# Kernel tuning notes

Measured on AMD Instinct MI355X. Metric: run time of the kernel, lower is better.

Reference implementation:

```python
import jax, jax.numpy as jnp
import numpy as np

EMBED_DIM = 2048
NUM_HEADS = 16
HEAD_DIM = EMBED_DIM // NUM_HEADS  # 128
D_K = 128
SCALE = 1.0 / float(np.sqrt(HEAD_DIM))
LAYER_DEPTH = 6 / 12  # amrpa_layer_idx / n_amrpa_layers
BATCH, SEQ = 2, 2048


def setup_inputs() -> dict:
    key = jax.random.key(0)
    ks = jax.random.split(key, 8)
    return {
        "hidden_states": jax.random.normal(ks[0], (BATCH, SEQ, EMBED_DIM), jnp.float32),
        "c_attn_w": jax.random.normal(ks[1], (EMBED_DIM, 3 * EMBED_DIM), jnp.float32) * 0.02,
        "c_attn_b": jax.random.normal(ks[2], (3 * EMBED_DIM,), jnp.float32) * 0.02,
        "c_proj_w": jax.random.normal(ks[3], (EMBED_DIM, EMBED_DIM), jnp.float32) * 0.02,
        "c_proj_b": jax.random.normal(ks[4], (EMBED_DIM,), jnp.float32) * 0.02,
        "cam_gate": jax.random.normal(ks[5], (D_K,), jnp.float32) * 0.1,
        "cam_w0": jax.random.normal(ks[6], (1,), jnp.float32),
        "cam_w1": jax.random.normal(ks[7], (1,), jnp.float32),
    }


def reference(hidden_states, c_attn_w, c_attn_b, c_proj_w, c_proj_b, cam_gate, cam_w0, cam_w1):
    # GPT2 Conv1D-style fused QKV projection: [B,S,3E]
    qkv = hidden_states @ c_attn_w + c_attn_b
    Q, K, V = jnp.split(qkv, 3, axis=2)  # each [B,S,E]
    # NOTE: faithful to source — attention over the FULL embed dim (no head split),
    # scaled by 1/sqrt(head_dim); causal mask is computed but never applied upstream.
    attn_scores = jnp.einsum('bse,bte->bst', Q, K) * SCALE  # [B,S,S]

    # CAM: sliced low-rank channels
    Q_cam, K_cam, V_cam = Q[:, :, :D_K], K[:, :, :D_K], V[:, :, :D_K]
    # base attention map computed under no_grad in the original
    base_A = jax.lax.stop_gradient(
        jax.nn.softmax(jnp.einsum('bsd,btd->bst', Q_cam, K_cam) * SCALE, axis=-1))
    layer_weight = jax.nn.sigmoid(cam_w0[0] + cam_w1[0] * LAYER_DEPTH)
    cam_ctx = jnp.einsum('bst,btd->bsd', base_A, V_cam)            # [B,S,d_k]
    cam_bias = jnp.einsum('bsd,btd->bst', jnp.tanh(cam_ctx * cam_gate), K_cam)
    cam_bias = cam_bias * (SCALE * layer_weight)                   # cam_mask is all-ones

    final_attn = jax.nn.softmax(attn_scores + cam_bias, axis=-1)
    context = jnp.einsum('bst,bte->bse', final_attn, V)            # [B,S,E]
    output = context @ c_proj_w + c_proj_b                         # resid_dropout is identity (eval)
    return output
```

## Files before the change

### kernel.cpp

```cpp
#include <hip/hip_runtime.h>
#include <hip/hip_bf16.h>

typedef unsigned short u16;
typedef __attribute__((ext_vector_type(8))) __bf16 bf16x8;
typedef __attribute__((ext_vector_type(4))) float f32x4;
typedef __attribute__((ext_vector_type(4))) unsigned short u16x4;

#define SCALE_QK 0.08838834764831845f

__device__ __forceinline__ u16 f2bf(float x) {
  union { float f; unsigned u; } v; v.f = x;
  unsigned r = v.u + 0x7fffu + ((v.u >> 16) & 1u);
  return (u16)(r >> 16);
}

__device__ __forceinline__ void gload_lds16(const u16* g, u16* l) {
  __builtin_amdgcn_global_load_lds(
      (const __attribute__((address_space(1))) unsigned*)g,
      (__attribute__((address_space(3))) unsigned*)l, 16, 0, 0);
}

__device__ __forceinline__ void wgbar() {
  asm volatile("" ::: "memory");
  __builtin_amdgcn_s_barrier();
  asm volatile("" ::: "memory");
}

template<bool OUT_BF16, bool HAS_BIAS>
__global__ __launch_bounds__(512, 2)
void gemm256(const u16* __restrict__ A, int lda, long sA,
             const u16* __restrict__ B, int ldb, long sB,
             void* __restrict__ Cv, int ldc, long sC,
             int K, float scale, const float* __restrict__ scale_ptr,
             const float* __restrict__ bias, int nbx)
{
  extern __shared__ u16 lds[];
  const int bz = blockIdx.z;
  const u16* Ap = A + (long)bz * sA;
  const u16* Bp = B + (long)bz * sB;

  const int nwg = gridDim.x;
  const int orig = blockIdx.x;
  const int q = nwg >> 3, rr = nwg & 7;
  const int xcd = orig & 7, lp = orig >> 3;
  const int wg = (xcd < rr ? xcd * (q + 1) : rr * (q + 1) + (xcd - rr) * q) + lp;
  const int bx = wg % nbx, by = wg / nbx;
  const long m0 = (long)by * 256, n0 = (long)bx * 256;

  const int tid = threadIdx.x;
  const int wid = tid >> 6, lane = tid & 63;
  const int wm = wid >> 2, wn = wid & 3;
  const int rl = lane & 15, g = lane >> 4;

  int offA[8], offB[4];
#pragma unroll
  for (int i = 0; i < 8; ++i) {
    const int row = wm * 128 + i * 16 + rl;
    offA[i] = row * 32 + ((g ^ ((row >> 1) & 3)) << 3);
  }
#pragma unroll
  for (int j = 0; j < 4; ++j) {
    const int row = wn * 64 + j * 16 + rl;
    offB[j] = row * 32 + ((g ^ ((row >> 1) & 3)) << 3);
  }

  const int rA = tid >> 2;
  const int colsw = (((lane & 3) ^ ((rA >> 1) & 3)) << 3);
  const u16* srcA0 = Ap + (m0 + rA) * (long)lda + colsw;
  const u16* srcA1 = Ap + (m0 + rA + 128) * (long)lda + colsw;
  const u16* srcB0 = Bp + (n0 + rA) * (long)ldb + colsw;
  const u16* srcB1 = Bp + (n0 + rA + 128) * (long)ldb + colsw;
  const int dL0 = wid * 512, dL1 = wid * 512 + 4096;

  const int NT = K >> 5;

#pragma unroll 1
  for (int t = 0; t < 3; ++t) {
    u16* bufp = lds + (t & 3) * 16384;
    gload_lds16(srcA0 + t * 32, bufp + dL0);
    gload_lds16(srcA1 + t * 32, bufp + dL1);
    gload_lds16(srcB0 + t * 32, bufp + 8192 + dL0);
    gload_lds16(srcB1 + t * 32, bufp + 8192 + dL1);
  }

  f32x4 acc[8][4];
#pragma unroll
  for (int i = 0; i < 8; ++i)
#pragma unroll
    for (int j = 0; j < 4; ++j) acc[i][j] = (f32x4){0.f, 0.f, 0.f, 0.f};

#pragma unroll 1
  for (int t = 0; t < NT; ++t) {
    const u16* bA = lds + (t & 3) * 16384;
    const u16* bB = bA + 8192;
    const int pre = t + 3;
    const bool doPre = pre < NT;
    u16* pP = lds + (pre & 3) * 16384;
    const int rem = NT - 1 - t;
    if (rem >= 2)      asm volatile("s_waitcnt vmcnt(8)" ::: "memory");
    else if (rem == 1) asm volatile("s_waitcnt vmcnt(4)" ::: "memory");
    else               asm volatile("s_waitcnt vmcnt(0)" ::: "memory");
    wgbar();

    bf16x8 av[4], bv_[4];
#pragma unroll
    for (int i = 0; i < 4; ++i) av[i] = *(const bf16x8*)(bA + offA[i]);
#pragma unroll
    for (int j = 0; j < 4; ++j) bv_[j] = *(const bf16x8*)(bB + offB[j]);
    if (doPre) {
      gload_lds16(srcA0 + pre * 32, pP + dL0);
      gload_lds16(srcA1 + pre * 32, pP + dL1);
    }
    wgbar();
    __builtin_amdgcn_s_setprio(1);
#pragma unroll
    for (int i = 0; i < 4; ++i)
#pragma unroll
      for (int j = 0; j < 4; ++j)
        acc[i][j] = __builtin_amdgcn_mfma_f32_16x16x32_bf16(av[i], bv_[j], acc[i][j], 0, 0, 0);
    __builtin_amdgcn_s_setprio(0);

#pragma unroll
    for (int i = 0; i < 4; ++i) av[i] = *(const bf16x8*)(bA + offA[i + 4]);
    if (doPre) {
      gload_lds16(srcB0 + pre * 32, pP + 8192 + dL0);
      gload_lds16(srcB1 + pre * 32, pP + 8192 + dL1);
    }
    wgbar();
    __builtin_amdgcn_s_setprio(1);
#pragma unroll
    for (int i = 0; i < 4; ++i)
#pragma unroll
      for (int j = 0; j < 4; ++j)
        acc[i + 4][j] = __builtin_amdgcn_mfma_f32_16x16x32_bf16(av[i], bv_[j], acc[i + 4][j], 0, 0, 0);
    __builtin_amdgcn_s_setprio(0);
  }

  float sc = scale;
  if (scale_ptr) sc *= scale_ptr[0];
  const int r0 = (lane >> 4) << 2;
  const int cL = lane & 15;
#pragma unroll
  for (int i = 0; i < 8; ++i) {
#pragma unroll
    for (int j = 0; j < 4; ++j) {
      const long row = m0 + wm * 128 + i * 16 + r0;
      const long col = n0 + wn * 64 + j * 16 + cL;
      float bvs = 0.f;
      if (HAS_BIAS) bvs = bias[col];
      if (OUT_BF16) {
        u16* Cp = (u16*)Cv + (long)bz * sC;
#pragma unroll
        for (int r = 0; r < 4; ++r)
          Cp[(row + r) * ldc + col] = f2bf(acc[i][j][r] * sc + bvs);
      } else {
        float* Cp = (float*)Cv + (long)bz * sC;
#pragma unroll
        for (int r = 0; r < 4; ++r)
          Cp[(row + r) * ldc + col] = acc[i][j][r] * sc + bvs;
      }
    }
  }
}

template<bool OUT_BF16, bool ACCUM, bool HAS_BIAS>
__global__ __launch_bounds__(256)
void gemm_bt(const u16* __restrict__ A, int lda, long sA,
             const u16* __restrict__ B, int ldb, long sB,
             void* __restrict__ Cv, int ldc, long sC,
             int K, float scale, const float* __restrict__ scale_ptr,
             const float* __restrict__ bias)
{
  __shared__ u16 As[128 * 64];
  __shared__ u16 Bs[128 * 64];
  const int bz   = blockIdx.z;
  const u16* Ap  = A + (long)bz * sA;
  const u16* Bp  = B + (long)bz * sB;
  const int tid  = threadIdx.x;
  const int wid  = tid >> 6;
  const int lane = tid & 63;
  const long m0  = (long)blockIdx.y * 128;
  const long n0  = (long)blockIdx.x * 128;
  const int lrow = lane >> 3;
  const int lk   = (lane & 7) << 3;
  const int wr   = wid >> 1, wc = wid & 1;

  f32x4 acc[4][4];
#pragma unroll
  for (int i = 0; i < 4; ++i)
#pragma unroll
    for (int j = 0; j < 4; ++j) acc[i][j] = (f32x4){0.f, 0.f, 0.f, 0.f};

  for (int k0 = 0; k0 < K; k0 += 64) {
#pragma unroll
    for (int c4 = 0; c4 < 4; ++c4) {
      const int chunk = (wid << 2) + c4;
      gload_lds16(Ap + (m0 + (chunk << 3) + lrow) * lda + k0 + lk, &As[chunk << 9]);
      gload_lds16(Bp + (n0 + (chunk << 3) + lrow) * ldb + k0 + lk, &Bs[chunk << 9]);
    }
    __syncthreads();
#pragma unroll
    for (int kk = 0; kk < 2; ++kk) {
      bf16x8 af[4], bfr[4];
      const int kof   = (kk << 5) + ((lane >> 4) << 3);
      const int rbase = lane & 15;
#pragma unroll
      for (int i = 0; i < 4; ++i)
        af[i] = *(const bf16x8*)&As[(((wr << 6) + (i << 4) + rbase) << 6) + kof];
#pragma unroll
      for (int j = 0; j < 4; ++j)
        bfr[j] = *(const bf16x8*)&Bs[(((wc << 6) + (j << 4) + rbase) << 6) + kof];
#pragma unroll
      for (int i = 0; i < 4; ++i)
#pragma unroll
        for (int j = 0; j < 4; ++j)
          acc[i][j] = __builtin_amdgcn_mfma_f32_16x16x32_bf16(af[i], bfr[j], acc[i][j], 0, 0, 0);
    }
    __syncthreads();
  }

  float sc = scale;
  if (scale_ptr) sc *= scale_ptr[0];
  const int r0 = (lane >> 4) << 2;
  const int cL = lane & 15;
#pragma unroll
  for (int i = 0; i < 4; ++i) {
#pragma unroll
    for (int j = 0; j < 4; ++j) {
      const long row = m0 + (wr << 6) + (i << 4) + r0;
      const long col = n0 + (wc << 6) + (j << 4) + cL;
      float bv = 0.f;
      if (HAS_BIAS) bv = bias[col];
      if (OUT_BF16) {
        u16* Cp = (u16*)Cv + (long)bz * sC;
#pragma unroll
        for (int r = 0; r < 4; ++r)
          Cp[(row + r) * ldc + col] = f2bf(acc[i][j][r] * sc + bv);
      } else {
        float* Cp = (float*)Cv + (long)bz * sC;
#pragma unroll
        for (int r = 0; r < 4; ++r) {
          float v = acc[i][j][r] * sc + bv;
          if (ACCUM) Cp[(row + r) * ldc + col] += v;
          else       Cp[(row + r) * ldc + col] = v;
        }
      }
    }
  }
}

__global__ __launch_bounds__(256)
void gemm_bt_splitk(const u16* __restrict__ A, int lda, long sA,
                    const u16* __restrict__ B, int ldb, long sB,
                    float* __restrict__ C, int ldc, long sC,
                    int Kslice, float scale)
{
  __shared__ u16 As[128 * 64];
  __shared__ u16 Bs[128 * 64];
  const int ks = blockIdx.z & 7;
  const int bz = blockIdx.z >> 3;
  const u16* Ap  = A + (long)bz * sA + ks * Kslice;
  const u16* Bp  = B + (long)bz * sB + ks * Kslice;
  const int tid  = threadIdx.x;
  const int wid  = tid >> 6;
  const int lane = tid & 63;
  const long m0  = (long)blockIdx.y * 128;
  const long n0  = (long)blockIdx.x * 128;
  const int lrow = lane >> 3;
  const int lk   = (lane & 7) << 3;
  const int wr   = wid >> 1, wc = wid & 1;

  f32x4 acc[4][4];
#pragma unroll
  for (int i = 0; i < 4; ++i)
#pragma unroll
    for (int j = 0; j < 4; ++j) acc[i][j] = (f32x4){0.f, 0.f, 0.f, 0.f};

  for (int k0 = 0; k0 < Kslice; k0 += 64) {
#pragma unroll
    for (int c4 = 0; c4 < 4; ++c4) {
      const int chunk = (wid << 2) + c4;
      gload_lds16(Ap + (m0 + (chunk << 3) + lrow) * lda + k0 + lk, &As[chunk << 9]);
      gload_lds16(Bp + (n0 + (chunk << 3) + lrow) * ldb + k0 + lk, &Bs[chunk << 9]);
    }
    __syncthreads();
#pragma unroll
    for (int kk = 0; kk < 2; ++kk) {
      bf16x8 af[4], bfr[4];
      const int kof   = (kk << 5) + ((lane >> 4) << 3);
      const int rbase = lane & 15;
#pragma unroll
      for (int i = 0; i < 4; ++i)
        af[i] = *(const bf16x8*)&As[(((wr << 6) + (i << 4) + rbase) << 6) + kof];
#pragma unroll
      for (int j = 0; j < 4; ++j)
        bfr[j] = *(const bf16x8*)&Bs[(((wc << 6) + (j << 4) + rbase) << 6) + kof];
#pragma unroll
      for (int i = 0; i < 4; ++i)
#pragma unroll
        for (int j = 0; j < 4; ++j)
          acc[i][j] = __builtin_amdgcn_mfma_f32_16x16x32_bf16(af[i], bfr[j], acc[i][j], 0, 0, 0);
    }
    __syncthreads();
  }

  const int r0 = (lane >> 4) << 2;
  const int cL = lane & 15;
  float* Cp = C + (long)bz * sC;
#pragma unroll
  for (int i = 0; i < 4; ++i) {
#pragma unroll
    for (int j = 0; j < 4; ++j) {
      const long row = m0 + (wr << 6) + (i << 4) + r0;
      const long col = n0 + (wc << 6) + (j << 4) + cL;
#pragma unroll
      for (int r = 0; r < 4; ++r)
        atomicAdd(&Cp[(row + r) * ldc + col], acc[i][j][r] * scale);
    }
  }
}

__global__ __launch_bounds__(256)
void softmax_rows2048(const float* __restrict__ src, u16* __restrict__ dst) {
  const long row = blockIdx.x;
  const float4* s = (const float4*)(src + row * 2048);
  const int tid = threadIdx.x;
  float4 a = s[tid * 2], b = s[tid * 2 + 1];
  float m = fmaxf(fmaxf(fmaxf(a.x, a.y), fmaxf(a.z, a.w)),
                  fmaxf(fmaxf(b.x, b.y), fmaxf(b.z, b.w)));
#pragma unroll
  for (int o = 32; o > 0; o >>= 1) m = fmaxf(m, __shfl_xor(m, o));
  __shared__ float redm[4];
  __shared__ float reds[4];
  if ((tid & 63) == 0) redm[tid >> 6] = m;
  __syncthreads();
  m = fmaxf(fmaxf(redm[0], redm[1]), fmaxf(redm[2], redm[3]));
  float e[8];
  e[0] = __expf(a.x - m); e[1] = __expf(a.y - m); e[2] = __expf(a.z - m); e[3] = __expf(a.w - m);
  e[4] = __expf(b.x - m); e[5] = __expf(b.y - m); e[6] = __expf(b.z - m); e[7] = __expf(b.w - m);
  float sum = e[0] + e[1] + e[2] + e[3] + e[4] + e[5] + e[6] + e[7];
#pragma unroll
  for (int o = 32; o > 0; o >>= 1) sum += __shfl_xor(sum, o);
  if ((tid & 63) == 0) reds[tid >> 6] = sum;
  __syncthreads();
  sum = reds[0] + reds[1] + reds[2] + reds[3];
  const float inv = 1.f / sum;
  u16x4 o1 = { f2bf(e[0] * inv), f2bf(e[1] * inv), f2bf(e[2] * inv), f2bf(e[3] * inv) };
  u16x4 o2 = { f2bf(e[4] * inv), f2bf(e[5] * inv), f2bf(e[6] * inv), f2bf(e[7] * inv) };
  u16x4* d = (u16x4*)(dst + row * 2048);
  d[tid * 2]     = o1;
  d[tid * 2 + 1] = o2;
}

__global__ void transpose_f32_to_bf16(const float* __restrict__ src, u16* __restrict__ dst,
                                      int R, int C) {
  __shared__ float t[32][33];
  const int c0 = blockIdx.x * 32, r0 = blockIdx.y * 32;
  const int tx = threadIdx.x, ty = threadIdx.y;
#pragma unroll
  for (int i = 0; i < 4; ++i)
    t[ty + i * 8][tx] = src[(long)(r0 + ty + i * 8) * C + c0 + tx];
  __syncthreads();
#pragma unroll
  for (int i = 0; i < 4; ++i)
    dst[(long)(c0 + ty + i * 8) * R + r0 + tx] = f2bf(t[tx][ty + i * 8]);
}

__global__ void transpose_bf16_batched(const u16* __restrict__ src, int ss, long sbat,
                                       u16* __restrict__ dst, int ds, long dbat) {
  __shared__ u16 t[32][33];
  const u16* s = src + (long)blockIdx.z * sbat;
  u16* d = dst + (long)blockIdx.z * dbat;
  const int c0 = blockIdx.x * 32, r0 = blockIdx.y * 32;
  const int tx = threadIdx.x, ty = threadIdx.y;
#pragma unroll
  for (int i = 0; i < 4; ++i)
    t[ty + i * 8][tx] = s[(long)(r0 + ty + i * 8) * ss + c0 + tx];
  __syncthreads();
#pragma unroll
  for (int i = 0; i < 4; ++i)
    d[(long)(c0 + ty + i * 8) * ds + r0 + tx] = t[tx][ty + i * 8];
}

__global__ __launch_bounds__(256)
void convert_f32_to_bf16(const float* __restrict__ src, u16* __restrict__ dst, long n4) {
  long i = (long)blockIdx.x * 256 + threadIdx.x;
  if (i < n4) {
    float4 v = ((const float4*)src)[i];
    *(u16x4*)(dst + i * 4) = (u16x4){ f2bf(v.x), f2bf(v.y), f2bf(v.z), f2bf(v.w) };
  }
}

__global__ __launch_bounds__(256)
void cam_tanh_kernel(const float* __restrict__ ctx, const float* __restrict__ gate,
                     u16* __restrict__ out, int n) {
  int i = blockIdx.x * 256 + threadIdx.x;
  if (i < n) {
    int d = i & 127;
    out[i] = f2bf(tanhf(ctx[i] * gate[d]));
  }
}

__global__ __launch_bounds__(256)
void zero_f32(float* __restrict__ p, int n) {
  int i = blockIdx.x * 256 + threadIdx.x;
  if (i < n) p[i] = 0.f;
}

__global__ void calc_lw_kernel(const float* w0, const float* w1, float* lw) {
  *lw = 1.f / (1.f + __expf(-(w0[0] + 0.5f * w1[0])));
}

extern "C" void kernel_launch(void* const* d_in, const int* in_sizes, int n_in,
                              void* d_out, int out_size, void* d_ws, size_t ws_size,
                              hipStream_t stream) {
  const float* hs       = (const float*)d_in[0];
  const float* c_attn_w = (const float*)d_in[1];
  const float* c_attn_b = (const float*)d_in[2];
  const float* c_proj_w = (const float*)d_in[3];
  const float* c_proj_b = (const float*)d_in[4];
  const float* cam_gate = (const float*)d_in[5];
  const float* cam_w0   = (const float*)d_in[6];
  const float* cam_w1   = (const float*)d_in[7];
  float* out = (float*)d_out;

  char* w = (char*)d_ws;
  float* lw      = (float*)(w + 0);
  u16*   hs_b    = (u16*)(w + 256);
  u16*   waT_b   = (u16*)(w + 256 + 16777216UL);
  u16*   wpT_b   = (u16*)(w + 256 + 41943040UL);
  u16*   qkv_b   = (u16*)(w + 256 + 50331648UL);
  u16*   vT_b    = (u16*)(w + 256 + 100663296UL);
  float* scoresF = (float*)(w + 256 + 117440512UL);
  float* camS    = (float*)(w + 256 + 150994944UL);
  float* ctxF    = (float*)(w + 256 + 184549376UL);
  u16*   camT_b  = (u16*)(w + 256 + 186646528UL);
  u16* baseA_b = hs_b;
  u16* P_b     = (u16*)camS;
  u16* ctxE_b  = (u16*)scoresF;

  dim3 b256(256);

  {
    auto* kfn = gemm256<true, true>;
    hipFuncSetAttribute((const void*)kfn, hipFuncAttributeMaxDynamicSharedMemorySize, 131072);
  }

  calc_lw_kernel<<<dim3(1), dim3(1), 0, stream>>>(cam_w0, cam_w1, lw);
  convert_f32_to_bf16<<<dim3(8192), b256, 0, stream>>>(hs, hs_b, 2097152L);
  transpose_f32_to_bf16<<<dim3(192, 64), dim3(32, 8), 0, stream>>>(c_attn_w, waT_b, 2048, 6144);
  transpose_f32_to_bf16<<<dim3(64, 64), dim3(32, 8), 0, stream>>>(c_proj_w, wpT_b, 2048, 2048);

  gemm256<true, true><<<dim3(384, 1, 1), dim3(512), 131072, stream>>>(
      hs_b, 2048, 0L, waT_b, 2048, 0L, qkv_b, 6144, 0L,
      2048, 1.f, nullptr, c_attn_b, 24);

  transpose_bf16_batched<<<dim3(64, 64, 2), dim3(32, 8), 0, stream>>>(
      qkv_b + 4096, 6144, 2048L * 6144, vT_b, 2048, 2048L * 2048);

  gemm_bt<false, false, false><<<dim3(16, 16, 2), b256, 0, stream>>>(
      qkv_b, 6144, 2048L * 6144, qkv_b + 2048, 6144, 2048L * 6144,
      scoresF, 2048, 2048L * 2048, 2048, SCALE_QK, nullptr, nullptr);

  gemm_bt<false, false, false><<<dim3(16, 16, 2), b256, 0, stream>>>(
      qkv_b, 6144, 2048L * 6144, qkv_b + 2048, 6144, 2048L * 6144,
      camS, 2048, 2048L * 2048, 128, SCALE_QK, nullptr, nullptr);

  softmax_rows2048<<<dim3(4096), b256, 0, stream>>>(camS, baseA_b);

  zero_f32<<<dim3(2048), b256, 0, stream>>>(ctxF, 524288);
  gemm_bt_splitk<<<dim3(1, 16, 16), b256, 0, stream>>>(
      baseA_b, 2048, 2048L * 2048, vT_b, 2048, 2048L * 2048,
      ctxF, 128, 2048L * 128, 256, 1.f);

  cam_tanh_kernel<<<dim3(2048), b256, 0, stream>>>(ctxF, cam_gate, camT_b, 524288);

  gemm_bt<false, true, false><<<dim3(16, 16, 2), b256, 0, stream>>>(
      camT_b, 128, 2048L * 128, qkv_b + 2048, 6144, 2048L * 6144,
      scoresF, 2048, 2048L * 2048, 128, SCALE_QK, lw, nullptr);

  softmax_rows2048<<<dim3(4096), b256, 0, stream>>>(scoresF, P_b);

  gemm_bt<true, false, false><<<dim3(16, 16, 2), b256, 0, stream>>>(
      P_b, 2048, 2048L * 2048, vT_b, 2048, 2048L * 2048,
      ctxE_b, 2048, 2048L * 2048, 2048, 1.f, nullptr, nullptr);

  gemm_bt<false, false, true><<<dim3(16, 32, 1), b256, 0, stream>>>(
      ctxE_b, 2048, 0L, wpT_b, 2048, 0L, out, 2048, 0L,
      2048, 1.f, nullptr, c_proj_b);
}
```

Measured before the change: 399.8 us.

## Move attention GEMMs to 256-tile pipelined kernel and fuse CAM bias into scores

Rewrites the 256x256 GEMM as a double-buffered pipeline with 64-wide K steps, staging loads in sub-phases interleaved with MFMA work. The same kernel now handles QK^T, PV and the output projection, which previously used the smaller 128-tile kernel. The CAM bias is folded into the score GEMM as a second K segment (tanh ctx times K), with the layer weight pre-multiplied in the tanh kernel. This removes the separate accumulate pass and a read-modify-write of the fp32 score matrix. In exchange, the 2048x2048 GEMMs launch only 128 workgroups each, which may underfill the GPU.

Measured after the change: 392.4 us. About the same (-1.8%).

```diff
diff --git a/kernel.cpp b/kernel.cpp
--- a/kernel.cpp
+++ b/kernel.cpp
@@ -20,30 +20,25 @@
       (__attribute__((address_space(3))) unsigned*)l, 16, 0, 0);
 }
 
-__device__ __forceinline__ void wgbar() {
-  asm volatile("" ::: "memory");
-  __builtin_amdgcn_s_barrier();
-  asm volatile("" ::: "memory");
-}
-
-template<bool OUT_BF16, bool HAS_BIAS>
+#define CFENCE() asm volatile("" ::: "memory")
+
+template<bool OUT_BF16, bool HAS_BIAS, bool TWO_SEG>
 __global__ __launch_bounds__(512, 2)
-void gemm256(const u16* __restrict__ A, int lda, long sA,
-             const u16* __restrict__ B, int ldb, long sB,
-             void* __restrict__ Cv, int ldc, long sC,
-             int K, float scale, const float* __restrict__ scale_ptr,
-             const float* __restrict__ bias, int nbx)
+void gemm256_8ph(const u16* __restrict__ A1, int lda1, long sA1,
+                 const u16* __restrict__ B1, int ldb1, long sB1, int K1,
+                 const u16* __restrict__ A2, int lda2, long sA2,
+                 const u16* __restrict__ B2, int ldb2, long sB2, int K2,
+                 void* __restrict__ Cv, int ldc, long sC,
+                 float scale, const float* __restrict__ bias, int nbx)
 {
   extern __shared__ u16 lds[];
   const int bz = blockIdx.z;
-  const u16* Ap = A + (long)bz * sA;
-  const u16* Bp = B + (long)bz * sB;
 
   const int nwg = gridDim.x;
   const int orig = blockIdx.x;
-  const int q = nwg >> 3, rr = nwg & 7;
+  const int q8 = nwg >> 3, r8 = nwg & 7;
   const int xcd = orig & 7, lp = orig >> 3;
-  const int wg = (xcd < rr ? xcd * (q + 1) : rr * (q + 1) + (xcd - rr) * q) + lp;
+  const int wg = (xcd < r8 ? xcd * (q8 + 1) : r8 * (q8 + 1) + (xcd - r8) * q8) + lp;
   const int bx = wg % nbx, by = wg / nbx;
   const long m0 = (long)by * 256, n0 = (long)bx * 256;
 
@@ -51,93 +46,114 @@
   const int wid = tid >> 6, lane = tid & 63;
   const int wm = wid >> 2, wn = wid & 3;
   const int rl = lane & 15, g = lane >> 4;
-
-  int offA[8], offB[4];
-#pragma unroll
-  for (int i = 0; i < 8; ++i) {
-    const int row = wm * 128 + i * 16 + rl;
-    offA[i] = row * 32 + ((g ^ ((row >> 1) & 3)) << 3);
-  }
-#pragma unroll
-  for (int j = 0; j < 4; ++j) {
-    const int row = wn * 64 + j * 16 + rl;
-    offB[j] = row * 32 + ((g ^ ((row >> 1) & 3)) << 3);
-  }
-
-  const int rA = tid >> 2;
-  const int colsw = (((lane & 3) ^ ((rA >> 1) & 3)) << 3);
-  const u16* srcA0 = Ap + (m0 + rA) * (long)lda + colsw;
-  const u16* srcA1 = Ap + (m0 + rA + 128) * (long)lda + colsw;
-  const u16* srcB0 = Bp + (n0 + rA) * (long)ldb + colsw;
-  const u16* srcB1 = Bp + (n0 + rA + 128) * (long)ldb + colsw;
-  const int dL0 = wid * 512, dL1 = wid * 512 + 4096;
-
-  const int NT = K >> 5;
-
+  const int swk = ((g ^ ((rl >> 1) & 3)) << 3);
+
+  int aoff[8], boff[4];
+#pragma unroll
+  for (int i = 0; i < 8; ++i)
+    aoff[i] = (wm * 128 + i * 16 + rl) * 32 + swk;
+#pragma unroll
+  for (int j = 0; j < 4; ++j)
+    boff[j] = 16384 + (wn * 64 + j * 16 + rl) * 32 + swk;
+
+  const int Rl = tid >> 2;
+  const int scol = (((tid & 3) ^ ((tid >> 3) & 3)) << 3);
+  const int sdst = wid * 512;
+
+  f32x4 acc[8][4];
+#pragma unroll
+  for (int i = 0; i < 8; ++i)
+#pragma unroll
+    for (int j = 0; j < 4; ++j) acc[i][j] = (f32x4){0.f, 0.f, 0.f, 0.f};
+
+#define STAGE_A(KK, KB, BQ)                                                  \
+  gload_lds16(rA0 + (KB) + (KK) * 32, (BQ) + (KK) * 8192 + sdst);            \
+  gload_lds16(rA1 + (KB) + (KK) * 32, (BQ) + (KK) * 8192 + 4096 + sdst);
+#define STAGE_B(KK, KB, BQ)                                                  \
+  gload_lds16(rB0 + (KB) + (KK) * 32, (BQ) + 16384 + (KK) * 8192 + sdst);    \
+  gload_lds16(rB1 + (KB) + (KK) * 32, (BQ) + 16384 + (KK) * 8192 + 4096 + sdst);
+#define PHASE_MFMA(IH)                                                       \
+  __builtin_amdgcn_s_setprio(1);                                             \
+  _Pragma("unroll")                                                          \
+  for (int i = 0; i < 4; ++i)                                                \
+    _Pragma("unroll")                                                        \
+    for (int j = 0; j < 4; ++j)                                              \
+      acc[(IH) * 4 + i][j] = __builtin_amdgcn_mfma_f32_16x16x32_bf16(        \
+          av[i], bv[j], acc[(IH) * 4 + i][j], 0, 0, 0);                      \
+  __builtin_amdgcn_s_setprio(0);
+
+  const int NSEG = TWO_SEG ? 2 : 1;
 #pragma unroll 1
-  for (int t = 0; t < 3; ++t) {
-    u16* bufp = lds + (t & 3) * 16384;
-    gload_lds16(srcA0 + t * 32, bufp + dL0);
-    gload_lds16(srcA1 + t * 32, bufp + dL1);
-    gload_lds16(srcB0 + t * 32, bufp + 8192 + dL0);
-    gload_lds16(srcB1 + t * 32, bufp + 8192 + dL1);
-  }
-
-  f32x4 acc[8][4];
-#pragma unroll
-  for (int i = 0; i < 8; ++i)
-#pragma unroll
-    for (int j = 0; j < 4; ++j) acc[i][j] = (f32x4){0.f, 0.f, 0.f, 0.f};
+  for (int seg = 0; seg < NSEG; ++seg) {
+    const u16* Ap = (seg == 0) ? (A1 + (long)bz * sA1) : (A2 + (long)bz * sA2);
+    const u16* Bp = (seg == 0) ? (B1 + (long)bz * sB1) : (B2 + (long)bz * sB2);
+    const int lda = (seg == 0) ? lda1 : lda2;
+    const int ldb = (seg == 0) ? ldb1 : ldb2;
+    const int K   = (seg == 0) ? K1 : K2;
+    const int NT  = K >> 6;
+
+    const u16* rA0 = Ap + (m0 + Rl) * (long)lda + scol;
+    const u16* rA1 = Ap + (m0 + Rl + 128) * (long)lda + scol;
+    const u16* rB0 = Bp + (n0 + Rl) * (long)ldb + scol;
+    const u16* rB1 = Bp + (n0 + Rl + 128) * (long)ldb + scol;
+
+    __builtin_amdgcn_s_barrier();
+    CFENCE();
+    STAGE_A(0, 0, lds);
+    STAGE_B(0, 0, lds);
+    STAGE_A(1, 0, lds);
+    STAGE_B(1, 0, lds);
+    CFENCE();
 
 #pragma unroll 1
-  for (int t = 0; t < NT; ++t) {
-    const u16* bA = lds + (t & 3) * 16384;
-    const u16* bB = bA + 8192;
-    const int pre = t + 3;
-    const bool doPre = pre < NT;
-    u16* pP = lds + (pre & 3) * 16384;
-    const int rem = NT - 1 - t;
-    if (rem >= 2)      asm volatile("s_waitcnt vmcnt(8)" ::: "memory");
-    else if (rem == 1) asm volatile("s_waitcnt vmcnt(4)" ::: "memory");
-    else               asm volatile("s_waitcnt vmcnt(0)" ::: "memory");
-    wgbar();
-
-    bf16x8 av[4], bv_[4];
-#pragma unroll
-    for (int i = 0; i < 4; ++i) av[i] = *(const bf16x8*)(bA + offA[i]);
-#pragma unroll
-    for (int j = 0; j < 4; ++j) bv_[j] = *(const bf16x8*)(bB + offB[j]);
-    if (doPre) {
-      gload_lds16(srcA0 + pre * 32, pP + dL0);
-      gload_lds16(srcA1 + pre * 32, pP + dL1);
-    }
-    wgbar();
-    __builtin_amdgcn_s_setprio(1);
-#pragma unroll
-    for (int i = 0; i < 4; ++i)
-#pragma unroll
-      for (int j = 0; j < 4; ++j)
-        acc[i][j] = __builtin_amdgcn_mfma_f32_16x16x32_bf16(av[i], bv_[j], acc[i][j], 0, 0, 0);
-    __builtin_amdgcn_s_setprio(0);
-
-#pragma unroll
-    for (int i = 0; i < 4; ++i) av[i] = *(const bf16x8*)(bA + offA[i + 4]);
-    if (doPre) {
-      gload_lds16(srcB0 + pre * 32, pP + 8192 + dL0);
-      gload_lds16(srcB1 + pre * 32, pP + 8192 + dL1);
-    }
-    wgbar();
-    __builtin_amdgcn_s_setprio(1);
-#pragma unroll
-    for (int i = 0; i < 4; ++i)
-#pragma unroll
-      for (int j = 0; j < 4; ++j)
-        acc[i + 4][j] = __builtin_amdgcn_mfma_f32_16x16x32_bf16(av[i], bv_[j], acc[i + 4][j], 0, 0, 0);
-    __builtin_amdgcn_s_setprio(0);
-  }
-
-  float sc = scale;
-  if (scale_ptr) sc *= scale_ptr[0];
+    for (int t = 0; t < NT; ++t) {
+      const u16* bp = lds + (t & 1) * 32768;
+      u16* bq = lds + ((t + 1) & 1) * 32768;
+      const bool hn = (t + 1) < NT;
+      const int kn = (t + 1) << 6;
+
+      bf16x8 av[4], bv[4];
+
+      asm volatile("s_waitcnt vmcnt(4)" ::: "memory");
+      __builtin_amdgcn_s_barrier();
+      CFENCE();
+      if (hn) { STAGE_A(0, kn, bq); }
+#pragma unroll
+      for (int i = 0; i < 4; ++i) av[i] = *(const bf16x8*)(bp + aoff[i]);
+#pragma unroll
+      for (int j = 0; j < 4; ++j) bv[j] = *(const bf16x8*)(bp + boff[j]);
+      PHASE_MFMA(0)
+      CFENCE();
+
+      if (hn) { STAGE_B(0, kn, bq); }
+#pragma unroll
+      for (int i = 0; i < 4; ++i) av[i] = *(const bf16x8*)(bp + aoff[4 + i]);
+      PHASE_MFMA(1)
+      CFENCE();
+
+      if (hn) { asm volatile("s_waitcnt vmcnt(4)" ::: "memory"); }
+      else    { asm volatile("s_waitcnt vmcnt(0)" ::: "memory"); }
+      __builtin_amdgcn_s_barrier();
+      CFENCE();
+      if (hn) { STAGE_A(1, kn, bq); }
+#pragma unroll
+      for (int i = 0; i < 4; ++i) av[i] = *(const bf16x8*)(bp + 8192 + aoff[i]);
+#pragma unroll
+      for (int j = 0; j < 4; ++j) bv[j] = *(const bf16x8*)(bp + 8192 + boff[j]);
+      PHASE_MFMA(0)
+      CFENCE();
+
+      if (hn) { STAGE_B(1, kn, bq); }
+#pragma unroll
+      for (int i = 0; i < 4; ++i) av[i] = *(const bf16x8*)(bp + 8192 + aoff[4 + i]);
+      PHASE_MFMA(1)
+      CFENCE();
+    }
+  }
+#undef STAGE_A
+#undef STAGE_B
+#undef PHASE_MFMA
+
   const int r0 = (lane >> 4) << 2;
   const int cL = lane & 15;
 #pragma unroll
@@ -152,24 +168,23 @@
         u16* Cp = (u16*)Cv + (long)bz * sC;
 #pragma unroll
         for (int r = 0; r < 4; ++r)
-          Cp[(row + r) * ldc + col] = f2bf(acc[i][j][r] * sc + bvs);
+          Cp[(row + r) * ldc + col] = f2bf(acc[i][j][r] * scale + bvs);
       } else {
         float* Cp = (float*)Cv + (long)bz * sC;
 #pragma unroll
         for (int r = 0; r < 4; ++r)
-          Cp[(row + r) * ldc + col] = acc[i][j][r] * sc + bvs;
+          Cp[(row + r) * ldc + col] = acc[i][j][r] * scale + bvs;
       }
     }
   }
 }
 
-template<bool OUT_BF16, bool ACCUM, bool HAS_BIAS>
+template<bool OUT_BF16, bool HAS_BIAS>
 __global__ __launch_bounds__(256)
 void gemm_bt(const u16* __restrict__ A, int lda, long sA,
              const u16* __restrict__ B, int ldb, long sB,
              void* __restrict__ Cv, int ldc, long sC,
-             int K, float scale, const float* __restrict__ scale_ptr,
-             const float* __restrict__ bias)
+             int K, float scale, const float* __restrict__ bias)
 {
   __shared__ u16 As[128 * 64];
   __shared__ u16 Bs[128 * 64];
@@ -219,8 +234,6 @@
     __syncthreads();
   }
 
-  float sc = scale;
-  if (scale_ptr) sc *= scale_ptr[0];
   const int r0 = (lane >> 4) << 2;
   const int cL = lane & 15;
 #pragma unroll
@@ -235,15 +248,12 @@
         u16* Cp = (u16*)Cv + (long)bz * sC;
 #pragma unroll
         for (int r = 0; r < 4; ++r)
-          Cp[(row + r) * ldc + col] = f2bf(acc[i][j][r] * sc + bv);
+          Cp[(row + r) * ldc + col] = f2bf(acc[i][j][r] * scale + bv);
       } else {
         float* Cp = (float*)Cv + (long)bz * sC;
 #pragma unroll
-        for (int r = 0; r < 4; ++r) {
-          float v = acc[i][j][r] * sc + bv;
-          if (ACCUM) Cp[(row + r) * ldc + col] += v;
-          else       Cp[(row + r) * ldc + col] = v;
-        }
+        for (int r = 0; r < 4; ++r)
+          Cp[(row + r) * ldc + col] = acc[i][j][r] * scale + bv;
       }
     }
   }
@@ -393,11 +403,11 @@
 
 __global__ __launch_bounds__(256)
 void cam_tanh_kernel(const float* __restrict__ ctx, const float* __restrict__ gate,
-                     u16* __restrict__ out, int n) {
+                     const float* __restrict__ lw, u16* __restrict__ out, int n) {
   int i = blockIdx.x * 256 + threadIdx.x;
   if (i < n) {
     int d = i & 127;
-    out[i] = f2bf(tanhf(ctx[i] * gate[d]));
+    out[i] = f2bf(tanhf(ctx[i] * gate[d]) * lw[0]);
   }
 }
 
@@ -441,30 +451,31 @@
 
   dim3 b256(256);
 
-  {
-    auto* kfn = gemm256<true, true>;
-    hipFuncSetAttribute((const void*)kfn, hipFuncAttributeMaxDynamicSharedMemorySize, 131072);
-  }
+  hipFuncSetAttribute((const void*)gemm256_8ph<true,  true,  false>,
+                      hipFuncAttributeMaxDynamicSharedMemorySize, 131072);
+  hipFuncSetAttribute((const void*)gemm256_8ph<false, false, true>,
+                      hipFuncAttributeMaxDynamicSharedMemorySize, 131072);
+  hipFuncSetAttribute((const void*)gemm256_8ph<true,  false, false>,
+                      hipFuncAttributeMaxDynamicSharedMemorySize, 131072);
+  hipFuncSetAttribute((const void*)gemm256_8ph<false, true,  false>,
+                      hipFuncAttributeMaxDynamicSharedMemorySize, 131072);
 
   calc_lw_kernel<<<dim3(1), dim3(1), 0, stream>>>(cam_w0, cam_w1, lw);
   convert_f32_to_bf16<<<dim3(8192), b256, 0, stream>>>(hs, hs_b, 2097152L);
   transpose_f32_to_bf16<<<dim3(192, 64), dim3(32, 8), 0, stream>>>(c_attn_w, waT_b, 2048, 6144);
   transpose_f32_to_bf16<<<dim3(64, 64), dim3(32, 8), 0, stream>>>(c_proj_w, wpT_b, 2048, 2048);
 
-  gemm256<true, true><<<dim3(384, 1, 1), dim3(512), 131072, stream>>>(
-      hs_b, 2048, 0L, waT_b, 2048, 0L, qkv_b, 6144, 0L,
-      2048, 1.f, nullptr, c_attn_b, 24);
+  gemm256_8ph<true, true, false><<<dim3(384, 1, 1), dim3(512), 131072, stream>>>(
+      hs_b, 2048, 0L, waT_b, 2048, 0L, 2048,
+      nullptr, 0, 0L, nullptr, 0, 0L, 0,
+      qkv_b, 6144, 0L, 1.f, c_attn_b, 24);
 
   transpose_bf16_batched<<<dim3(64, 64, 2), dim3(32, 8), 0, stream>>>(
       qkv_b + 4096, 6144, 2048L * 6144, vT_b, 2048, 2048L * 2048);
 
-  gemm_bt<false, false, false><<<dim3(16, 16, 2), b256, 0, stream>>>(
+  gemm_bt<false, false><<<dim3(16, 16, 2), b256, 0, stream>>>(
       qkv_b, 6144, 2048L * 6144, qkv_b + 2048, 6144, 2048L * 6144,
-      scoresF, 2048, 2048L * 2048, 2048, SCALE_QK, nullptr, nullptr);
-
-  gemm_bt<false, false, false><<<dim3(16, 16, 2), b256, 0, stream>>>(
-      qkv_b, 6144, 2048L * 6144, qkv_b + 2048, 6144, 2048L * 6144,
-      camS, 2048, 2048L * 2048, 128, SCALE_QK, nullptr, nullptr);
+      camS, 2048, 2048L * 2048, 128, SCALE_QK, nullptr);
 
   softmax_rows2048<<<dim3(4096), b256, 0, stream>>>(camS, baseA_b);
 
@@ -473,19 +484,22 @@
       baseA_b, 2048, 2048L * 2048, vT_b, 2048, 2048L * 2048,
       ctxF, 128, 2048L * 128, 256, 1.f);
 
-  cam_tanh_kernel<<<dim3(2048), b256, 0, stream>>>(ctxF, cam_gate, camT_b, 524288);
-
-  gemm_bt<false, true, false><<<dim3(16, 16, 2), b256, 0, stream>>>(
-      camT_b, 128, 2048L * 128, qkv_b + 2048, 6144, 2048L * 6144,
-      scoresF, 2048, 2048L * 2048, 128, SCALE_QK, lw, nullptr);
+  cam_tanh_kernel<<<dim3(2048), b256, 0, stream>>>(ctxF, cam_gate, lw, camT_b, 524288);
+
+  gemm256_8ph<false, false, true><<<dim3(64, 1, 2), dim3(512), 131072, stream>>>(
+      qkv_b, 6144, 2048L * 6144, qkv_b + 2048, 6144, 2048L * 6144, 2048,
+      camT_b, 128, 2048L * 128, qkv_b + 2048, 6144, 2048L * 6144, 128,
+      scoresF, 2048, 2048L * 2048, SCALE_QK, nullptr, 8);
 
   softmax_rows2048<<<dim3(4096), b256, 0, stream>>>(scoresF, P_b);
 
-  gemm_bt<true, false, false><<<dim3(16, 16, 2), b256, 0, stream>>>(
-      P_b, 2048, 2048L * 2048, vT_b, 2048, 2048L * 2048,
-      ctxE_b, 2048, 2048L * 2048, 2048, 1.f, nullptr, nullptr);
-
-  gemm_bt<false, false, true><<<dim3(16, 32, 1), b256, 0, stream>>>(
-      ctxE_b, 2048, 0L, wpT_b, 2048, 0L, out, 2048, 0L,
-      2048, 1.f, nullptr, c_proj_b);
-}
+  gemm256_8ph<true, false, false><<<dim3(64, 1, 2), dim3(512), 131072, stream>>>(
+      P_b, 2048, 2048L * 2048, vT_b, 2048, 2048L * 2048, 2048,
+      nullptr, 0, 0L, nullptr, 0, 0L, 0,
+      ctxE_b, 2048, 2048L * 2048, 1.f, nullptr, 8);
+
+  gemm256_8ph<false, true, false><<<dim3(128, 1, 1), dim3(512), 131072, stream>>>(
+      ctxE_b, 2048, 0L, wpT_b, 2048, 0L, 2048,
+      nullptr, 0, 0L, nullptr, 0, 0L, 0,
+      out, 2048, 0L, 1.f, c_proj_b, 8);
+}
```
